# Kernel tuning notes

Measured on AMD Instinct MI355X. Metric: run time of the kernel, lower is better.

Reference implementation:

```python
import jax, jax.numpy as jnp
import numpy as np

BIG = 1e6
EPS = 1e-12


def _normalize(x):
    return x / (jnp.linalg.norm(x, axis=-1, keepdims=True) + EPS)


def _euclidean_dist(x, y):
    # x: [m, d], y: [n, d] -> [m, n]
    xx = jnp.sum(x * x, axis=1, keepdims=True)          # [m, 1]
    yy = jnp.sum(y * y, axis=1)[None, :]                # [1, n]
    d = xx + yy - 2.0 * (x @ y.T)
    return jnp.sqrt(jnp.clip(d, EPS, None))


def _cam_loss(embeddings, labels, centers_value, centers_cnt, margin):
    B, D = embeddings.shape
    C = centers_value.shape[0]

    # --- _Cup: centroid scatter-reduce update (detached in original) ---
    emb_d = jax.lax.stop_gradient(embeddings)
    sums = jax.ops.segment_sum(emb_d, labels, num_segments=C)              # [C, D]
    counts = jax.ops.segment_sum(jnp.ones((B,), emb_d.dtype), labels,
                                 num_segments=C)                           # [C]
    upd_val = jax.lax.stop_gradient(centers_value) + sums
    upd_cnt = jax.lax.stop_gradient(centers_cnt) + counts[:, None]
    centers = jnp.where(upd_cnt > 0, upd_val / jnp.maximum(upd_cnt, 1.0), 0.0)

    centers = _normalize(centers)
    emb = _normalize(embeddings)

    pd = _euclidean_dist(emb, emb)        # [B, B]
    pdc = _euclidean_dist(emb, centers)   # [B, C]

    # masks
    eye = jnp.eye(B, dtype=bool)
    labels_eq = labels[None, :] == labels[:, None]
    mask_ap = (~eye) & labels_eq          # anchor-positive [B, B]
    mask_an = ~labels_eq                  # anchor-negative [B, B]
    classes = jnp.arange(C)
    mask_ap_c = labels[:, None] == classes[None, :]   # [B, C]
    mask_an_c = ~mask_ap_c

    # hardest positive
    hp = jnp.max(mask_ap * pd, axis=1, keepdims=True)
    hp_c = jnp.max(mask_ap_c * pdc, axis=1, keepdims=True)
    hpos = jnp.maximum(hp, hp_c)                       # [B, 1]
    hpos_d = jax.lax.stop_gradient(hpos)

    # hardest negative: outside the positive boundary
    greater = pd > hpos_d
    greater_c = pdc > hpos_d
    gbm = mask_an & greater
    gbm_c = mask_an_c & greater_c
    neg_out = jnp.min(pd + BIG * (~gbm), axis=1, keepdims=True)
    neg_out_c = jnp.min(pdc + BIG * (~gbm_c), axis=1, keepdims=True)
    h_out = jnp.minimum(neg_out, neg_out_c)

    # hardest negative: inside (rows with no negative beyond the boundary)
    ms = jnp.sum(gbm, axis=1) == 0        # [B]
    ms_c = jnp.sum(gbm_c, axis=1) == 0
    neg_in = jnp.max(jnp.where(ms[:, None], pd, BIG) * mask_an,
                     axis=1, keepdims=True)
    neg_in_c = jnp.max(jnp.where(ms_c[:, None], pdc, BIG) * mask_an_c,
                       axis=1, keepdims=True)
    h_in = jnp.maximum(neg_in, neg_in_c)

    hneg = jnp.minimum(h_out, h_in)       # [B, 1]

    # MarginRankingLoss(dist_an, dist_ap, y=1, reduction='sum') / B
    loss = jnp.sum(jax.nn.relu(hpos - hneg + margin)) / B
    return loss


def setup_inputs() -> dict:
    key = jax.random.key(0)
    k1, k2 = jax.random.split(key)
    B, D, C = 4096, 2048, 1024
    return {
        "embeddings": jax.random.normal(k1, (B, D), dtype=jnp.float32),
        "labels": jax.random.randint(k2, (B,), 0, C),
        "centers_value": jnp.zeros((C, D), dtype=jnp.float32),
        "centers_cnt": jnp.zeros((C, D), dtype=jnp.float32),
        "margin": jnp.float32(1.0),
    }


def reference(embeddings, labels, centers_value, centers_cnt, margin):
    return _cam_loss(embeddings, labels, centers_value, centers_cnt, margin)
```

## Files before the change

### kernel.cpp

```cpp
#include <hip/hip_runtime.h>
#include <hip/hip_bf16.h>


typedef __attribute__((ext_vector_type(8))) short short8;
typedef __attribute__((ext_vector_type(4))) float f32x4;

#define BIGF 1e6f
#define EPSC 1e-12f

__device__ __forceinline__ float bf2f(unsigned short u){
  unsigned int x = ((unsigned int)u) << 16;
  return __uint_as_float(x);
}
__device__ __forceinline__ unsigned short f2bf(float f){
  __hip_bfloat16 h = __float2bfloat16(f);
  return *reinterpret_cast<unsigned short*>(&h);
}

__device__ __forceinline__ float block_reduce_sum(float v){
  __shared__ float red[4];
  int tid = threadIdx.x;
  __syncthreads();
  #pragma unroll
  for (int s = 32; s; s >>= 1) v += __shfl_xor(v, s);
  if ((tid & 63) == 0) red[tid >> 6] = v;
  __syncthreads();
  return red[0] + red[1] + red[2] + red[3];
}

#define GLL16(gptr, lptr) \
  __builtin_amdgcn_global_load_lds( \
      (const __attribute__((address_space(1))) unsigned int*)(gptr), \
      (__attribute__((address_space(3))) unsigned int*)(lptr), 16, 0, 0)

#define VMWAIT(S) asm volatile("s_waitcnt " S ::: "memory")
#define SBAR()    asm volatile("s_barrier" ::: "memory")

__global__ __launch_bounds__(256) void k_setup(const int* __restrict__ labels,
    int* cnt, int* members,
    unsigned* mn0, unsigned* mx0, unsigned* fl0,
    unsigned* mn1, unsigned* mx1, unsigned* fl1,
    int B, int C, int MMAX){
  int gid = blockIdx.x * blockDim.x + threadIdx.x;
  unsigned bigbits = __float_as_uint(BIGF);
  if (gid < B){
    mn0[gid] = bigbits; mx0[gid] = 0u; fl0[gid] = 0u;
    mn1[gid] = bigbits; mx1[gid] = 0u; fl1[gid] = 0u;
  }
  int w = threadIdx.x >> 6, lane = threadIdx.x & 63;
  int c = blockIdx.x * 4 + w;
  if (c >= C) return;
  int base = 0;
  int nit = (B + 63) >> 6;
  for (int itc = 0; itc < nit; ++itc){
    int idx = itc * 64 + lane;
    int lab = (idx < B) ? labels[idx] : -1;
    unsigned long long m = __ballot(lab == c);
    if (lab == c){
      int rk = base + (int)__popcll(m & ((1ull << lane) - 1ull));
      if (rk < MMAX) members[c * MMAX + rk] = idx;
    }
    base += (int)__popcll(m);
  }
  if (lane == 0) cnt[c] = base;
}

template<int R>
__global__ __launch_bounds__(256) void k_prep(const float* __restrict__ emb,
    const float* __restrict__ cval, const float* __restrict__ ccnt,
    const int* __restrict__ cnt, const int* __restrict__ members,
    unsigned short* __restrict__ enb, unsigned short* __restrict__ cnb,
    float* __restrict__ exx, float* __restrict__ cxx,
    int D, int MMAX, int nbNorm){
  int w = threadIdx.x >> 6, lane = threadIdx.x & 63;
  if ((int)blockIdx.x < nbNorm){
    int i = blockIdx.x * 4 + w;
    const float* row = emb + (size_t)i * D;
    float v[R][8];
    float ss = 0.f;
    #pragma unroll
    for (int r = 0; r < R; ++r){
      int base = r * 512 + lane * 8;
      float4 a = *reinterpret_cast<const float4*>(&row[base]);
      float4 b = *reinterpret_cast<const float4*>(&row[base + 4]);
      v[r][0]=a.x; v[r][1]=a.y; v[r][2]=a.z; v[r][3]=a.w;
      v[r][4]=b.x; v[r][5]=b.y; v[r][6]=b.z; v[r][7]=b.w;
      #pragma unroll
      for (int k = 0; k < 8; ++k) ss += v[r][k] * v[r][k];
    }
    #pragma unroll
    for (int s = 1; s < 64; s <<= 1) ss += __shfl_xor(ss, s);
    float inv = 1.f / (sqrtf(ss) + EPSC);
    unsigned short* orow = enb + (size_t)i * D;
    int xr = (i & 7) << 3;
    #pragma unroll
    for (int r = 0; r < R; ++r){
      int base = (r * 512 + lane * 8) ^ xr;
      short8 o;
      #pragma unroll
      for (int k = 0; k < 8; ++k) o[k] = (short)f2bf(v[r][k] * inv);
      *reinterpret_cast<short8*>(&orow[base]) = o;
    }
    if (lane == 0) exx[i] = ss * inv * inv;
  } else {
    int c = ((int)blockIdx.x - nbNorm) * 4 + w;
    int n = cnt[c], m = n < MMAX ? n : MMAX;
    float acc[R][8];
    #pragma unroll
    for (int r = 0; r < R; ++r)
      #pragma unroll
      for (int k = 0; k < 8; ++k) acc[r][k] = 0.f;
    for (int e = 0; e < m; ++e){
      const float* row = emb + (size_t)members[c * MMAX + e] * D;
      #pragma unroll
      for (int r = 0; r < R; ++r){
        int base = r * 512 + lane * 8;
        float4 a = *reinterpret_cast<const float4*>(&row[base]);
        float4 b = *reinterpret_cast<const float4*>(&row[base + 4]);
        acc[r][0]+=a.x; acc[r][1]+=a.y; acc[r][2]+=a.z; acc[r][3]+=a.w;
        acc[r][4]+=b.x; acc[r][5]+=b.y; acc[r][6]+=b.z; acc[r][7]+=b.w;
      }
    }
    float cf = (float)n;
    float ss = 0.f;
    #pragma unroll
    for (int r = 0; r < R; ++r){
      int base = r * 512 + lane * 8;
      float4 u0 = *reinterpret_cast<const float4*>(&ccnt[(size_t)c * D + base]);
      float4 u1 = *reinterpret_cast<const float4*>(&ccnt[(size_t)c * D + base + 4]);
      float4 w0 = *reinterpret_cast<const float4*>(&cval[(size_t)c * D + base]);
      float4 w1 = *reinterpret_cast<const float4*>(&cval[(size_t)c * D + base + 4]);
      float uc[8] = {u0.x,u0.y,u0.z,u0.w,u1.x,u1.y,u1.z,u1.w};
      float wv[8] = {w0.x,w0.y,w0.z,w0.w,w1.x,w1.y,w1.z,w1.w};
      #pragma unroll
      for (int k = 0; k < 8; ++k){
        float u = uc[k] + cf;
        float vv = wv[k] + acc[r][k];
        float ce = (u > 0.f) ? (vv / fmaxf(u, 1.f)) : 0.f;
        acc[r][k] = ce; ss += ce * ce;
      }
    }
    #pragma unroll
    for (int s = 1; s < 64; s <<= 1) ss += __shfl_xor(ss, s);
    float inv = 1.f / (sqrtf(ss) + EPSC);
    int xr = (c & 7) << 3;
    #pragma unroll
    for (int r = 0; r < R; ++r){
      int base = (r * 512 + lane * 8) ^ xr;
      short8 o;
      #pragma unroll
      for (int k = 0; k < 8; ++k) o[k] = (short)f2bf(acc[r][k] * inv);
      *reinterpret_cast<short8*>(&cnb[(size_t)c * D + base]) = o;
    }
    if (lane == 0) cxx[c] = ss * inv * inv;
  }
}

template<int NCH>
__global__ __launch_bounds__(256) void k_hpos(const unsigned short* __restrict__ enb,
    const unsigned short* __restrict__ cnb, const float* __restrict__ exx,
    const float* __restrict__ cxx, const int* __restrict__ labels,
    const int* __restrict__ cnt, const int* __restrict__ members,
    float* __restrict__ hpos, int D, int MMAX){
  int w = threadIdx.x >> 6, lane = threadIdx.x & 63;
  int i = blockIdx.x * 4 + w;
  int li = labels[i];
  const unsigned short* arow = enb + (size_t)i * D;
  int xri = (i & 7) << 3;
  float av[NCH][8];
  #pragma unroll
  for (int ch = 0; ch < NCH; ++ch){
    short8 a8 = *reinterpret_cast<const short8*>(&arow[(ch * 512 + lane * 8) ^ xri]);
    #pragma unroll
    for (int k = 0; k < 8; ++k) av[ch][k] = bf2f((unsigned short)a8[k]);
  }
  float xi = exx[i];
  float hp = 0.f;
  int m = cnt[li] < MMAX ? cnt[li] : MMAX;
  for (int e = 0; e < m; ++e){
    int j = members[li * MMAX + e];
    if (j == i) continue;
    const unsigned short* brow = enb + (size_t)j * D;
    int xrj = (j & 7) << 3;
    float p = 0.f;
    #pragma unroll
    for (int ch = 0; ch < NCH; ++ch){
      short8 b8 = *reinterpret_cast<const short8*>(&brow[(ch * 512 + lane * 8) ^ xrj]);
      #pragma unroll
      for (int k = 0; k < 8; ++k) p += av[ch][k] * bf2f((unsigned short)b8[k]);
    }
    #pragma unroll
    for (int s = 1; s < 64; s <<= 1) p += __shfl_xor(p, s);
    float d2 = xi + exx[j] - 2.f * p;
    hp = fmaxf(hp, sqrtf(fmaxf(d2, EPSC)));
  }
  {
    const unsigned short* brow = cnb + (size_t)li * D;
    int xrc = (li & 7) << 3;
    float p = 0.f;
    #pragma unroll
    for (int ch = 0; ch < NCH; ++ch){
      short8 b8 = *reinterpret_cast<const short8*>(&brow[(ch * 512 + lane * 8) ^ xrc]);
      #pragma unroll
      for (int k = 0; k < 8; ++k) p += av[ch][k] * bf2f((unsigned short)b8[k]);
    }
    #pragma unroll
    for (int s = 1; s < 64; s <<= 1) p += __shfl_xor(p, s);
    float d2 = xi + cxx[li] - 2.f * p;
    hp = fmaxf(hp, sqrtf(fmaxf(d2, EPSC)));
  }
  if (lane == 0) hpos[i] = hp;
}

#define PD_STAGE(SB, KIND, KT) do { \
    unsigned short* dst_ = (SB) + (KIND) * 8192 + wid * (16 * 64); \
    const unsigned short* src_ = ((KIND) < 2 \
        ? gA + (size_t)((KIND) * 128) * D \
        : gB + (size_t)(((KIND) - 2) * 128) * D) + (KT); \
    GLL16(src_, dst_); \
    GLL16(src_ + (size_t)8 * D, dst_ + 8 * 64); \
  } while (0)

#define RD_A(DST, HP) do { \
    _Pragma("unroll") \
    for (int m_ = 0; m_ < 4; ++m_){ \
      DST[m_][0] = *reinterpret_cast<const short8*>(&(HP)[aoff[m_][0]]); \
      DST[m_][1] = *reinterpret_cast<const short8*>(&(HP)[aoff[m_][1]]); \
    } } while (0)

#define RD_B(HP) do { \
    _Pragma("unroll") \
    for (int n_ = 0; n_ < 2; ++n_){ \
      b[n_][0] = *reinterpret_cast<const short8*>(&(HP)[boff[n_][0]]); \
      b[n_][1] = *reinterpret_cast<const short8*>(&(HP)[boff[n_][1]]); \
    } } while (0)

#define LGKM0() do { VMWAIT("lgkmcnt(0)"); __builtin_amdgcn_sched_barrier(0); } while (0)

#define MFMA16(AV, MH, NH) do { \
    __builtin_amdgcn_s_setprio(1); \
    _Pragma("unroll") \
    for (int m_ = 0; m_ < 4; ++m_) \
      _Pragma("unroll") \
      for (int n_ = 0; n_ < 2; ++n_) \
        _Pragma("unroll") \
        for (int ks_ = 0; ks_ < 2; ++ks_) \
          acc[MH][NH][m_][n_] = __builtin_amdgcn_mfma_f32_16x16x32_bf16( \
              AV[m_][ks_], b[n_][ks_], acc[MH][NH][m_][n_], 0, 0, 0); \
    __builtin_amdgcn_s_setprio(0); } while (0)

__global__ __launch_bounds__(512, 2) void k_pd_all(
    const unsigned short* __restrict__ enb,
    const unsigned short* __restrict__ cnb,
    const float* __restrict__ exx, const float* __restrict__ cxx,
    const int* __restrict__ labels, const float* __restrict__ hpos,
    unsigned* __restrict__ mn0, unsigned* __restrict__ mx0, unsigned* __restrict__ fl0,
    unsigned* __restrict__ mn1, unsigned* __restrict__ mx1, unsigned* __restrict__ fl1,
    int D, int nTri, int nby, int nCx)
{
  extern __shared__ unsigned short sm[];
  const int nwg = gridDim.x;
  const int orig = blockIdx.x;
  const int q8 = nwg >> 3, r8 = nwg & 7;
  const int xcd = orig & 7, idx = orig >> 3;
  const int t = (xcd < r8 ? xcd * (q8 + 1) : r8 * (q8 + 1) + (xcd - r8) * q8) + idx;

  const bool pdc = (t >= nTri);
  int bx, by;
  if (!pdc){
    if ((nby & 3) == 0){
      int gb = 0, cb = 0, rem = t;
      for (;;){
        int sz = (cb < gb) ? 16 : 10;
        if (rem < sz) break;
        rem -= sz;
        if (++cb > gb){ cb = 0; ++gb; }
      }
      if (cb < gb){
        by = gb * 4 + (rem >> 2);
        bx = cb * 4 + (rem & 3);
      } else {
        int r = 0;
        while (((r + 1) * (r + 2)) / 2 <= rem) ++r;
        by = gb * 4 + r;
        bx = cb * 4 + (rem - (r * (r + 1)) / 2);
      }
    } else {
      int b_ = (int)((sqrtf(8.f * (float)t + 1.f) - 1.f) * 0.5f);
      while ((b_ + 1) * (b_ + 2) / 2 <= t) ++b_;
      while (b_ * (b_ + 1) / 2 > t) --b_;
      by = b_; bx = t - b_ * (b_ + 1) / 2;
    }
  } else {
    int u = t - nTri;
    by = u / nCx; bx = u - by * nCx;
  }
  const unsigned short* cmat = pdc ? cnb : enb;
  const float* cxv = pdc ? cxx : exx;
  unsigned* mnv = pdc ? mn1 : mn0;
  unsigned* mxv = pdc ? mx1 : mx0;
  unsigned* flv = pdc ? fl1 : fl0;

  const int j0 = bx * 256, i0 = by * 256;
  const int tid = threadIdx.x;
  const int wid = tid >> 6, lane = tid & 63;
  const int wr = wid >> 2, wc = wid & 3;
  const int lr = lane & 15, lg = lane >> 4;

  const int srow = wid * 16 + (lane >> 3);
  const int scol = (lane & 7) * 8;
  const unsigned short* gA = enb  + (size_t)(i0 + srow) * D + scol;
  const unsigned short* gB = cmat + (size_t)(j0 + srow) * D + scol;

  int aoff[4][2], boff[2][2];
  #pragma unroll
  for (int m = 0; m < 4; ++m){
    int ra = wr * 64 + m * 16 + lr;
    #pragma unroll
    for (int ks = 0; ks < 2; ++ks)
      aoff[m][ks] = ra * 64 + ((ks * 32 + lg * 8) ^ ((ra & 7) << 3));
  }
  #pragma unroll
  for (int n = 0; n < 2; ++n){
    int rb = wc * 32 + n * 16 + lr;
    #pragma unroll
    for (int ks = 0; ks < 2; ++ks)
      boff[n][ks] = rb * 64 + ((ks * 32 + lg * 8) ^ ((rb & 7) << 3));
  }

  f32x4 acc[2][2][4][2];
  #pragma unroll
  for (int mh = 0; mh < 2; ++mh)
    #pragma unroll
    for (int nh = 0; nh < 2; ++nh)
      #pragma unroll
      for (int m = 0; m < 4; ++m)
        #pragma unroll
        for (int n = 0; n < 2; ++n)
          acc[mh][nh][m][n] = (f32x4){0.f, 0.f, 0.f, 0.f};

  short8 a0[4][2], a1[4][2], b[2][2];

  const int nt = D >> 6;
  PD_STAGE(sm, 0, 0); PD_STAGE(sm, 1, 0); PD_STAGE(sm, 2, 0); PD_STAGE(sm, 3, 0);
  VMWAIT("vmcnt(0)");
  SBAR();

  for (int it = 0; it < nt; ++it){
    const unsigned short* db = sm + (size_t)(it & 1) * 32768;
    unsigned short* sb = sm + (size_t)((it & 1) ^ 1) * 32768;
    const bool hn = (it + 1 < nt);
    const int ktn = (it + 1) << 6;
    RD_A(a0, db);
    RD_B(db + 2 * 8192);
    if (hn){ PD_STAGE(sb, 0, ktn); VMWAIT("vmcnt(4)"); } else { VMWAIT("vmcnt(4)"); }
    SBAR();
    LGKM0();
    MFMA16(a0, 0, 0);
    RD_A(a1, db + 8192);
    if (hn){ PD_STAGE(sb, 2, ktn); VMWAIT("vmcnt(4)"); } else { VMWAIT("vmcnt(2)"); }
    SBAR();
    LGKM0();
    MFMA16(a1, 1, 0);
    RD_B(db + 3 * 8192);
    if (hn){ PD_STAGE(sb, 1, ktn); VMWAIT("vmcnt(4)"); } else { VMWAIT("vmcnt(0)"); }
    SBAR();
    LGKM0();
    MFMA16(a1, 1, 1);
    if (hn){ PD_STAGE(sb, 3, ktn); VMWAIT("vmcnt(4)"); }
    SBAR();
    MFMA16(a0, 0, 1);
  }

  const bool docol = (!pdc) && (bx != by);
  int jl[2][2]; float xj[2][2], hpj[2][2];
  #pragma unroll
  for (int nh = 0; nh < 2; ++nh)
    #pragma unroll
    for (int n = 0; n < 2; ++n){
      int j = j0 + nh * 128 + wc * 32 + n * 16 + lr;
      jl[nh][n] = pdc ? j : labels[j];
      xj[nh][n] = cxv[j];
      hpj[nh][n] = docol ? hpos[j] : 0.f;
    }
  float cmn[2][2], cmx[2][2]; int cfl[2][2];
  #pragma unroll
  for (int nh = 0; nh < 2; ++nh)
    #pragma unroll
    for (int n = 0; n < 2; ++n){ cmn[nh][n] = BIGF; cmx[nh][n] = 0.f; cfl[nh][n] = 0; }

  #pragma unroll
  for (int mh = 0; mh < 2; ++mh)
    #pragma unroll
    for (int m = 0; m < 4; ++m)
      #pragma unroll
      for (int r = 0; r < 4; ++r){
        int i = i0 + mh * 128 + wr * 64 + m * 16 + lg * 4 + r;
        int li = labels[i];
        float xi = exx[i];
        float hpi = hpos[i];
        float mn = BIGF, mx = 0.f; int fl = 0;
        #pragma unroll
        for (int nh = 0; nh < 2; ++nh)
          #pragma unroll
          for (int n = 0; n < 2; ++n){
            float d2 = xi + xj[nh][n] - 2.f * acc[mh][nh][m][n][r];
            float d  = sqrtf(fmaxf(d2, EPSC));
            bool an = (li != jl[nh][n]);
            bool g  = an && (d > hpi);
            mn = fminf(mn, g ? d : BIGF);
            mx = fmaxf(mx, an ? d : 0.f);
            fl |= (g ? 1 : 0) | (an ? 2 : 0);
            if (docol){
              bool gc = an && (d > hpj[nh][n]);
              cmn[nh][n] = fminf(cmn[nh][n], gc ? d : BIGF);
              cmx[nh][n] = fmaxf(cmx[nh][n], an ? d : 0.f);
              cfl[nh][n] |= (gc ? 1 : 0) | (an ? 2 : 0);
            }
          }
        #pragma unroll
        for (int s = 1; s < 16; s <<= 1){
          mn = fminf(mn, __shfl_xor(mn, s));
          mx = fmaxf(mx, __shfl_xor(mx, s));
          fl |= __shfl_xor(fl, s);
        }
        if (lr == 0){
          atomicMin(&mnv[i], __float_as_uint(mn));
          atomicMax(&mxv[i], __float_as_uint(mx));
          if (fl) atomicOr(&flv[i], (unsigned)fl);
        }
      }
  if (docol){
    #pragma unroll
    for (int nh = 0; nh < 2; ++nh)
      #pragma unroll
      for (int n = 0; n < 2; ++n){
        float mn = cmn[nh][n], mx = cmx[nh][n]; int fl = cfl[nh][n];
        #pragma unroll
        for (int s = 16; s < 64; s <<= 1){
          mn = fminf(mn, __shfl_xor(mn, s));
          mx = fmaxf(mx, __shfl_xor(mx, s));
          fl |= __shfl_xor(fl, s);
        }
        if (lg == 0){
          int j = j0 + nh * 128 + wc * 32 + n * 16 + lr;
          atomicMin(&mn0[j], __float_as_uint(mn));
          atomicMax(&mx0[j], __float_as_uint(mx));
          if (fl) atomicOr(&fl0[j], (unsigned)fl);
        }
      }
  }
}

__global__ __launch_bounds__(256) void k_final(const float* __restrict__ hpos,
    const unsigned* __restrict__ mn0, const unsigned* __restrict__ mx0,
    const unsigned* __restrict__ fl0, const unsigned* __restrict__ mn1,
    const unsigned* __restrict__ mx1, const unsigned* __restrict__ fl1,
    const float* __restrict__ margin, float* __restrict__ out, int B){
  float part = 0.f;
  float mar = margin[0];
  for (int i = threadIdx.x; i < B; i += blockDim.x){
    float h_out = fminf(__uint_as_float(mn0[i]), __uint_as_float(mn1[i]));
    unsigned f0 = fl0[i], f1 = fl1[i];
    float ni  = (!(f0 & 1u)) ? __uint_as_float(mx0[i]) : ((f0 & 2u) ? BIGF : 0.f);
    float nic = (!(f1 & 1u)) ? __uint_as_float(mx1[i]) : ((f1 & 2u) ? BIGF : 0.f);
    float h_in = fmaxf(ni, nic);
    float hneg = fminf(h_out, h_in);
    float t = hpos[i] - hneg + mar;
    part += fmaxf(t, 0.f);
  }
  float tot = block_reduce_sum(part);
  if (threadIdx.x == 0) out[0] = tot / (float)B;
}

extern "C" void kernel_launch(void* const* d_in, const int* in_sizes, int n_in,
                              void* d_out, int out_size, void* d_ws, size_t ws_size,
                              hipStream_t stream){
  const float* emb    = (const float*)d_in[0];
  const int*   labels = (const int*)d_in[1];
  const float* cval   = (const float*)d_in[2];
  const float* ccnt   = (const float*)d_in[3];
  const float* margin = (const float*)d_in[4];
  float* out = (float*)d_out;

  int B = in_sizes[1];
  int D = in_sizes[0] / B;
  int C = in_sizes[2] / D;
  const int MMAX = 64;

  char* ws = (char*)d_ws;
  size_t off = 0;
  auto alloc = [&](size_t bytes)->char*{
    char* p = ws + off;
    off = (off + bytes + 255) & ~(size_t)255;
    return p;
  };
  unsigned short* enb = (unsigned short*)alloc((size_t)B * D * 2);
  unsigned short* cnb = (unsigned short*)alloc((size_t)C * D * 2);
  float* exx  = (float*)alloc((size_t)B * 4);
  float* cxx  = (float*)alloc((size_t)C * 4);
  float* hpos = (float*)alloc((size_t)B * 4);
  unsigned* mn0 = (unsigned*)alloc((size_t)B * 4);
  unsigned* mx0 = (unsigned*)alloc((size_t)B * 4);
  unsigned* fl0 = (unsigned*)alloc((size_t)B * 4);
  unsigned* mn1 = (unsigned*)alloc((size_t)B * 4);
  unsigned* mx1 = (unsigned*)alloc((size_t)B * 4);
  unsigned* fl1 = (unsigned*)alloc((size_t)B * 4);
  int* cnt     = (int*)alloc((size_t)C * 4);
  int* members = (int*)alloc((size_t)C * MMAX * 4);
  (void)ws_size; (void)n_in; (void)out_size;

  hipFuncSetAttribute((const void*)k_pd_all,
                      hipFuncAttributeMaxDynamicSharedMemorySize, 131072);

  int nbSetup = (C + 3) / 4;
  int nbInit  = ((B > C ? B : C) + 255) / 256;
  if (nbInit > nbSetup) nbSetup = nbInit;
  k_setup<<<nbSetup, 256, 0, stream>>>(labels, cnt, members,
                                       mn0, mx0, fl0, mn1, mx1, fl1, B, C, MMAX);

  int nbNorm = B / 4, nbCent = C / 4;
  int R = D >> 9;
  if (R == 4){
    k_prep<4><<<nbNorm + nbCent, 256, 0, stream>>>(emb, cval, ccnt, cnt, members,
                                                   enb, cnb, exx, cxx, D, MMAX, nbNorm);
  } else if (R == 2){
    k_prep<2><<<nbNorm + nbCent, 256, 0, stream>>>(emb, cval, ccnt, cnt, members,
                                                   enb, cnb, exx, cxx, D, MMAX, nbNorm);
  } else {
    k_prep<1><<<nbNorm + nbCent, 256, 0, stream>>>(emb, cval, ccnt, cnt, members,
                                                   enb, cnb, exx, cxx, D, MMAX, nbNorm);
  }

  switch (R){
    case 1: k_hpos<1><<<B/4, 256, 0, stream>>>(enb, cnb, exx, cxx, labels, cnt, members, hpos, D, MMAX); break;
    case 2: k_hpos<2><<<B/4, 256, 0, stream>>>(enb, cnb, exx, cxx, labels, cnt, members, hpos, D, MMAX); break;
    default: k_hpos<4><<<B/4, 256, 0, stream>>>(enb, cnb, exx, cxx, labels, cnt, members, hpos, D, MMAX); break;
  }

  int nby = B / 256, nCx = C / 256;
  int nTri = nby * (nby + 1) / 2;
  k_pd_all<<<nTri + nby * nCx, 512, 131072, stream>>>(
      enb, cnb, exx, cxx, labels, hpos,
      mn0, mx0, fl0, mn1, mx1, fl1, D, nTri, nby, nCx);
  k_final<<<1, 256, 0, stream>>>(hpos, mn0, mx0, fl0, mn1, mx1, fl1, margin, out, B);
}
```

Measured before the change: 153.7 us.

## Compute hardest-positive per class with shared member rows and symmetric dot products

Replaces the per-anchor hardest-positive kernel with a per-class kernel in which one wavefront loads every member row of a class once. For classes with up to 8 members it computes all pairwise dot products plus each member's dot with the centroid in registers, using symmetry so each pair is computed once. Larger classes fall back to a per-member loop. The goal is to cut redundant global loads and dot products. The costs are higher register pressure, and per-class work imbalance with fewer waves (C/4 blocks instead of B/4). hpos is now zero-initialized in setup so classes that are skipped leave defined values.

```diff
diff --git a/kernel.cpp b/kernel.cpp
--- a/kernel.cpp
+++ b/kernel.cpp
@@ -37,7 +37,7 @@
 #define SBAR()    asm volatile("s_barrier" ::: "memory")
 
 __global__ __launch_bounds__(256) void k_setup(const int* __restrict__ labels,
-    int* cnt, int* members,
+    int* cnt, int* members, float* hpos,
     unsigned* mn0, unsigned* mx0, unsigned* fl0,
     unsigned* mn1, unsigned* mx1, unsigned* fl1,
     int B, int C, int MMAX){
@@ -46,6 +46,7 @@
   if (gid < B){
     mn0[gid] = bigbits; mx0[gid] = 0u; fl0[gid] = 0u;
     mn1[gid] = bigbits; mx1[gid] = 0u; fl1[gid] = 0u;
+    hpos[gid] = 0.f;
   }
   int w = threadIdx.x >> 6, lane = threadIdx.x & 63;
   int c = blockIdx.x * 4 + w;
@@ -156,60 +157,142 @@
   }
 }
 
-template<int NCH>
-__global__ __launch_bounds__(256) void k_hpos(const unsigned short* __restrict__ enb,
-    const unsigned short* __restrict__ cnb, const float* __restrict__ exx,
-    const float* __restrict__ cxx, const int* __restrict__ labels,
+template<int R>
+__global__ __launch_bounds__(256) void k_hpos_class(
+    const unsigned short* __restrict__ enb, const unsigned short* __restrict__ cnb,
+    const float* __restrict__ exx, const float* __restrict__ cxx,
     const int* __restrict__ cnt, const int* __restrict__ members,
-    float* __restrict__ hpos, int D, int MMAX){
-  int w = threadIdx.x >> 6, lane = threadIdx.x & 63;
-  int i = blockIdx.x * 4 + w;
-  int li = labels[i];
-  const unsigned short* arow = enb + (size_t)i * D;
-  int xri = (i & 7) << 3;
-  float av[NCH][8];
-  #pragma unroll
-  for (int ch = 0; ch < NCH; ++ch){
-    short8 a8 = *reinterpret_cast<const short8*>(&arow[(ch * 512 + lane * 8) ^ xri]);
-    #pragma unroll
-    for (int k = 0; k < 8; ++k) av[ch][k] = bf2f((unsigned short)a8[k]);
-  }
-  float xi = exx[i];
-  float hp = 0.f;
-  int m = cnt[li] < MMAX ? cnt[li] : MMAX;
-  for (int e = 0; e < m; ++e){
-    int j = members[li * MMAX + e];
-    if (j == i) continue;
-    const unsigned short* brow = enb + (size_t)j * D;
-    int xrj = (j & 7) << 3;
-    float p = 0.f;
-    #pragma unroll
-    for (int ch = 0; ch < NCH; ++ch){
-      short8 b8 = *reinterpret_cast<const short8*>(&brow[(ch * 512 + lane * 8) ^ xrj]);
-      #pragma unroll
-      for (int k = 0; k < 8; ++k) p += av[ch][k] * bf2f((unsigned short)b8[k]);
-    }
-    #pragma unroll
-    for (int s = 1; s < 64; s <<= 1) p += __shfl_xor(p, s);
-    float d2 = xi + exx[j] - 2.f * p;
-    hp = fmaxf(hp, sqrtf(fmaxf(d2, EPSC)));
-  }
-  {
-    const unsigned short* brow = cnb + (size_t)li * D;
-    int xrc = (li & 7) << 3;
-    float p = 0.f;
-    #pragma unroll
-    for (int ch = 0; ch < NCH; ++ch){
-      short8 b8 = *reinterpret_cast<const short8*>(&brow[(ch * 512 + lane * 8) ^ xrc]);
-      #pragma unroll
-      for (int k = 0; k < 8; ++k) p += av[ch][k] * bf2f((unsigned short)b8[k]);
-    }
-    #pragma unroll
-    for (int s = 1; s < 64; s <<= 1) p += __shfl_xor(p, s);
-    float d2 = xi + cxx[li] - 2.f * p;
-    hp = fmaxf(hp, sqrtf(fmaxf(d2, EPSC)));
-  }
-  if (lane == 0) hpos[i] = hp;
+    float* __restrict__ hpos, int D, int MMAX, int C){
+  int wid = threadIdx.x >> 6, lane = threadIdx.x & 63;
+  int c = blockIdx.x * 4 + wid;
+  if (c >= C) return;
+  int m = cnt[c]; if (m > MMAX) m = MMAX;
+  if (m == 0) return;
+  float xc = cxx[c];
+  int xrc = (c & 7) << 3;
+  const unsigned short* crow = cnb + (size_t)c * D;
+
+  if (m <= 8){
+    int idx[8]; float xx[8]; int xr[8];
+    const unsigned short* rows[8];
+    #pragma unroll
+    for (int e = 0; e < 8; ++e){
+      if (e < m){
+        idx[e] = members[c * MMAX + e];
+        xx[e] = exx[idx[e]];
+        rows[e] = enb + (size_t)idx[e] * D;
+        xr[e] = (idx[e] & 7) << 3;
+      }
+    }
+    float ap[8][8];
+    #pragma unroll
+    for (int e1 = 0; e1 < 8; ++e1)
+      #pragma unroll
+      for (int e2 = e1; e2 < 8; ++e2) ap[e1][e2] = 0.f;
+    for (int ch = 0; ch < R; ++ch){
+      int base = ch * 512 + lane * 8;
+      float rc[8];
+      {
+        short8 v = *reinterpret_cast<const short8*>(&crow[base ^ xrc]);
+        #pragma unroll
+        for (int k = 0; k < 8; ++k) rc[k] = bf2f((unsigned short)v[k]);
+      }
+      float r[8][8];
+      #pragma unroll
+      for (int e = 0; e < 8; ++e){
+        if (e < m){
+          short8 v = *reinterpret_cast<const short8*>(&rows[e][base ^ xr[e]]);
+          #pragma unroll
+          for (int k = 0; k < 8; ++k) r[e][k] = bf2f((unsigned short)v[k]);
+        }
+      }
+      #pragma unroll
+      for (int e1 = 0; e1 < 8; ++e1){
+        if (e1 < m){
+          #pragma unroll
+          for (int k = 0; k < 8; ++k) ap[e1][e1] += r[e1][k] * rc[k];
+          #pragma unroll
+          for (int e2 = e1 + 1; e2 < 8; ++e2){
+            if (e2 < m){
+              #pragma unroll
+              for (int k = 0; k < 8; ++k) ap[e1][e2] += r[e1][k] * r[e2][k];
+            }
+          }
+        }
+      }
+    }
+    #pragma unroll
+    for (int e1 = 0; e1 < 8; ++e1)
+      #pragma unroll
+      for (int e2 = e1; e2 < 8; ++e2){
+        float v = ap[e1][e2];
+        #pragma unroll
+        for (int s = 1; s < 64; s <<= 1) v += __shfl_xor(v, s);
+        ap[e1][e2] = v;
+      }
+    #pragma unroll
+    for (int e1 = 0; e1 < 8; ++e1){
+      if (e1 < m){
+        float d2c = xx[e1] + xc - 2.f * ap[e1][e1];
+        float hp = sqrtf(fmaxf(d2c, EPSC));
+        #pragma unroll
+        for (int e2 = 0; e2 < 8; ++e2){
+          if (e2 < m && e2 != e1){
+            float dot = (e2 > e1) ? ap[e1][e2] : ap[e2][e1];
+            float dd = xx[e1] + xx[e2] - 2.f * dot;
+            hp = fmaxf(hp, sqrtf(fmaxf(dd, EPSC)));
+          }
+        }
+        if (lane == 0) hpos[idx[e1]] = hp;
+      }
+    }
+  } else {
+    for (int e1 = 0; e1 < m; ++e1){
+      int i = members[c * MMAX + e1];
+      const unsigned short* arow = enb + (size_t)i * D;
+      int xri = (i & 7) << 3;
+      float av[R][8];
+      #pragma unroll
+      for (int ch = 0; ch < R; ++ch){
+        short8 v = *reinterpret_cast<const short8*>(&arow[(ch * 512 + lane * 8) ^ xri]);
+        #pragma unroll
+        for (int k = 0; k < 8; ++k) av[ch][k] = bf2f((unsigned short)v[k]);
+      }
+      float xi = exx[i];
+      float hp;
+      {
+        float p = 0.f;
+        #pragma unroll
+        for (int ch = 0; ch < R; ++ch){
+          short8 v = *reinterpret_cast<const short8*>(&crow[(ch * 512 + lane * 8) ^ xrc]);
+          #pragma unroll
+          for (int k = 0; k < 8; ++k) p += av[ch][k] * bf2f((unsigned short)v[k]);
+        }
+        #pragma unroll
+        for (int s = 1; s < 64; s <<= 1) p += __shfl_xor(p, s);
+        float d2 = xi + xc - 2.f * p;
+        hp = sqrtf(fmaxf(d2, EPSC));
+      }
+      for (int e2 = 0; e2 < m; ++e2){
+        if (e2 == e1) continue;
+        int j = members[c * MMAX + e2];
+        const unsigned short* brow = enb + (size_t)j * D;
+        int xrj = (j & 7) << 3;
+        float p = 0.f;
+        #pragma unroll
+        for (int ch = 0; ch < R; ++ch){
+          short8 v = *reinterpret_cast<const short8*>(&brow[(ch * 512 + lane * 8) ^ xrj]);
+          #pragma unroll
+          for (int k = 0; k < 8; ++k) p += av[ch][k] * bf2f((unsigned short)v[k]);
+        }
+        #pragma unroll
+        for (int s = 1; s < 64; s <<= 1) p += __shfl_xor(p, s);
+        float d2 = xi + exx[j] - 2.f * p;
+        hp = fmaxf(hp, sqrtf(fmaxf(d2, EPSC)));
+      }
+      if (lane == 0) hpos[i] = hp;
+    }
+  }
 }
 
 #define PD_STAGE(SB, KIND, KT) do { \
@@ -516,7 +599,7 @@
   int nbSetup = (C + 3) / 4;
   int nbInit  = ((B > C ? B : C) + 255) / 256;
   if (nbInit > nbSetup) nbSetup = nbInit;
-  k_setup<<<nbSetup, 256, 0, stream>>>(labels, cnt, members,
+  k_setup<<<nbSetup, 256, 0, stream>>>(labels, cnt, members, hpos,
                                        mn0, mx0, fl0, mn1, mx1, fl1, B, C, MMAX);
 
   int nbNorm = B / 4, nbCent = C / 4;
@@ -524,18 +607,18 @@
   if (R == 4){
     k_prep<4><<<nbNorm + nbCent, 256, 0, stream>>>(emb, cval, ccnt, cnt, members,
                                                    enb, cnb, exx, cxx, D, MMAX, nbNorm);
+    k_hpos_class<4><<<(C + 3) / 4, 256, 0, stream>>>(enb, cnb, exx, cxx, cnt, members,
+                                                     hpos, D, MMAX, C);
   } else if (R == 2){
     k_prep<2><<<nbNorm + nbCent, 256, 0, stream>>>(emb, cval, ccnt, cnt, members,
                                                    enb, cnb, exx, cxx, D, MMAX, nbNorm);
+    k_hpos_class<2><<<(C + 3) / 4, 256, 0, stream>>>(enb, cnb, exx, cxx, cnt, members,
+                                                     hpos, D, MMAX, C);
   } else {
     k_prep<1><<<nbNorm + nbCent, 256, 0, stream>>>(emb, cval, ccnt, cnt, members,
                                                    enb, cnb, exx, cxx, D, MMAX, nbNorm);
-  }
-
-  switch (R){
-    case 1: k_hpos<1><<<B/4, 256, 0, stream>>>(enb, cnb, exx, cxx, labels, cnt, members, hpos, D, MMAX); break;
-    case 2: k_hpos<2><<<B/4, 256, 0, stream>>>(enb, cnb, exx, cxx, labels, cnt, members, hpos, D, MMAX); break;
-    default: k_hpos<4><<<B/4, 256, 0, stream>>>(enb, cnb, exx, cxx, labels, cnt, members, hpos, D, MMAX); break;
+    k_hpos_class<1><<<(C + 3) / 4, 256, 0, stream>>>(enb, cnb, exx, cxx, cnt, members,
+                                                     hpos, D, MMAX, C);
   }
 
   int nby = B / 256, nCx = C / 256;
```

Measured after the change: 219.0 us. +42.5%, slower.
